# Kernel tuning notes

Measured on AMD Instinct MI355X. Metric: run time of the kernel, lower is better.

## Reference

```python
import jax, jax.numpy as jnp
import numpy as np
import math

D_MODEL = 1024
NUM_HEADS = 16
HEAD_DIM = D_MODEL // NUM_HEADS
B, T = 2, 2048


def _linear_params(key, d_in, d_out):
    kw, kb = jax.random.split(key)
    s = 1.0 / math.sqrt(d_in)
    W = jax.random.uniform(kw, (d_in, d_out), jnp.float32, -s, s)
    b = jax.random.uniform(kb, (d_out,), jnp.float32, -s, s)
    return W, b


def setup_inputs() -> dict:
    key = jax.random.key(0)
    ks = jax.random.split(key, 10)
    x_real = jax.random.normal(ks[0], (B, T, D_MODEL), jnp.float32)
    x_imag = jax.random.normal(ks[1], (B, T, D_MODEL), jnp.float32)
    Wqr, bqr = _linear_params(ks[2], D_MODEL, D_MODEL)
    Wqi, bqi = _linear_params(ks[3], D_MODEL, D_MODEL)
    Wkr, bkr = _linear_params(ks[4], D_MODEL, D_MODEL)
    Wki, bki = _linear_params(ks[5], D_MODEL, D_MODEL)
    Wvr, bvr = _linear_params(ks[6], D_MODEL, D_MODEL)
    Wvi, bvi = _linear_params(ks[7], D_MODEL, D_MODEL)
    Wor, bor = _linear_params(ks[8], D_MODEL, D_MODEL)
    Woi, boi = _linear_params(ks[9], D_MODEL, D_MODEL)
    return dict(x_real=x_real, x_imag=x_imag,
                Wqr=Wqr, bqr=bqr, Wqi=Wqi, bqi=bqi,
                Wkr=Wkr, bkr=bkr, Wki=Wki, bki=bki,
                Wvr=Wvr, bvr=bvr, Wvi=Wvi, bvi=bvi,
                Wor=Wor, bor=bor, Woi=Woi, boi=boi)


def _heads(x):
    # (B,T,C) -> (B,H,T,Dh)
    b, t, _ = x.shape
    return x.reshape(b, t, NUM_HEADS, HEAD_DIM).transpose(0, 2, 1, 3)


def reference(x_real, x_imag,
              Wqr, bqr, Wqi, bqi, Wkr, bkr, Wki, bki,
              Wvr, bvr, Wvi, bvi, Wor, bor, Woi, boi):
    b, t, c = x_real.shape
    # NOTE: first two qr/qi assignments in the torch forward are dead code;
    # effective math is below.
    qr = _heads(x_real @ Wqr + bqr)
    qi = _heads(x_imag @ Wqi + bqi)
    kr = _heads(x_real @ Wkr + bkr)
    ki = _heads(x_imag @ Wki + bki)
    vr = _heads(x_real @ Wvr + bvr)
    vi = _heads(x_imag @ Wvi + bvi)
    # Re(Q K^H) score: Qr*Kr + Qi*Ki, scaled
    score = (jnp.einsum('bhtd,bhsd->bhts', qr, kr)
             + jnp.einsum('bhtd,bhsd->bhts', qi, ki)) / math.sqrt(HEAD_DIM)
    causal = jnp.triu(jnp.ones((t, t), dtype=bool), k=1)  # True above diagonal
    score = jnp.where(causal[None, None], -jnp.inf, score)
    attn = jax.nn.softmax(score, axis=-1)
    out_r = jnp.einsum('bhts,bhsd->bhtd', attn, vr).transpose(0, 2, 1, 3).reshape(b, t, c)
    out_i = jnp.einsum('bhts,bhsd->bhtd', attn, vi).transpose(0, 2, 1, 3).reshape(b, t, c)
    final_r = out_r @ Wor + bor
    final_i = out_i @ Woi + boi
    return (final_r, final_i)
```

## Files before the change

kernel.cpp:

```cpp
#include <hip/hip_runtime.h>
#include <hip/hip_bf16.h>


typedef __attribute__((ext_vector_type(8))) __bf16 bf16x8;
typedef __attribute__((ext_vector_type(4))) float f32x4;
typedef unsigned short u16;

#define L2E 1.44269504088896340736f

__device__ __forceinline__ void gl2lds16(const void* g, void* l) {
  __builtin_amdgcn_global_load_lds(
      (const __attribute__((address_space(1))) unsigned int*)g,
      (__attribute__((address_space(3))) unsigned int*)l, 16, 0, 0);
}

__device__ __forceinline__ u16 f2bf(float f) {
  union { float f; unsigned u; } v;
  v.f = f;
  unsigned r = v.u + 0x7FFFu + ((v.u >> 16) & 1u);
  return (u16)(r >> 16);
}

__global__ void cvt_bf16_2(const float* __restrict__ a, const float* __restrict__ bsrc,
                           u16* __restrict__ oa, u16* __restrict__ ob, int n) {
  const float* in = blockIdx.y ? bsrc : a;
  u16* out = blockIdx.y ? ob : oa;
  int stride = gridDim.x * blockDim.x * 4;
  for (int i = (blockIdx.x * blockDim.x + threadIdx.x) * 4; i < n; i += stride) {
    float4 v = *(const float4*)(in + i);
    ushort4 o;
    o.x = f2bf(v.x); o.y = f2bf(v.y); o.z = f2bf(v.z); o.w = f2bf(v.w);
    *(ushort4*)(out + i) = o;
  }
}

struct WPtrs { const float* w[8]; };

__global__ void cvt_w_t(WPtrs ptrs, u16* __restrict__ out) {
  __shared__ float tile[32][33];
  const float* W = ptrs.w[blockIdx.z];
  u16* o = out + ((size_t)blockIdx.z << 20);
  int tx = threadIdx.x & 31, ty = threadIdx.x >> 5;
  int bx = blockIdx.x * 32, by = blockIdx.y * 32;
#pragma unroll
  for (int k = 0; k < 4; k++) {
    int r = by + ty + k * 8;
    tile[ty + k * 8][tx] = W[(size_t)r * 1024 + bx + tx];
  }
  __syncthreads();
#pragma unroll
  for (int k = 0; k < 4; k++) {
    int n = bx + ty + k * 8;
    o[(size_t)n * 1024 + by + tx] = f2bf(tile[tx][ty + k * 8]);
  }
}

struct GemmArgs {
  const u16* A[6];
  const u16* Wt[6];
  const float* bias[6];
  void* dst[6];
  int off[6];
  int vt[6];
  float scale[6];
};

template <int MODE>
__global__ __launch_bounds__(256, 2) void gemm_bf16(GemmArgs args) {
  extern __shared__ u16 dynpad[];
  const int z = blockIdx.z;
  const u16* __restrict__ A = args.A[z];
  const u16* __restrict__ Bt = args.Wt[z];
  const float* __restrict__ bias = args.bias[z];
  const int brow = blockIdx.x * 128;
  const int bcol = blockIdx.y * 128;

  __shared__ u16 smem[2][2][128 * 32];

  const int tid = threadIdx.x;
  const int w = tid >> 6, lane = tid & 63;
  const int ql = lane & 15, hi = lane >> 4;
  const int wrow = (w >> 1) * 64, wcol = (w & 1) * 64;

  if (args.off[z] == -12345) ((volatile u16*)dynpad)[0] = 0;

  f32x4 acc[4][4] = {};

  auto stage = [&](int buf, int t) {
    int k0 = t * 32;
#pragma unroll
    for (int s = 0; s < 2; s++) {
      int q = w * 2 + s;
      int lr = q * 16 + (lane >> 2);
      int csrc = (lane & 3) ^ ((lr >> 1) & 3);
      gl2lds16(A + (size_t)(brow + lr) * 1024 + k0 + csrc * 8, &smem[0][buf][q * 512]);
    }
#pragma unroll
    for (int s = 0; s < 2; s++) {
      int q = w * 2 + s;
      int lr = q * 16 + (lane >> 2);
      int csrc = (lane & 3) ^ ((lr >> 1) & 3);
      gl2lds16(Bt + (size_t)(bcol + lr) * 1024 + k0 + csrc * 8, &smem[1][buf][q * 512]);
    }
  };

  stage(0, 0);
  __syncthreads();

  int buf = 0;
  for (int t = 0; t < 32; t++) {
    if (t + 1 < 32) stage(buf ^ 1, t + 1);
    bf16x8 a[4], b[4];
#pragma unroll
    for (int i = 0; i < 4; i++) {
      int row = wrow + i * 16 + ql;
      int cs = hi ^ ((row >> 1) & 3);
      a[i] = *(const bf16x8*)&smem[0][buf][row * 32 + cs * 8];
      int col = wcol + i * 16 + ql;
      int cs2 = hi ^ ((col >> 1) & 3);
      b[i] = *(const bf16x8*)&smem[1][buf][col * 32 + cs2 * 8];
    }
#pragma unroll
    for (int i = 0; i < 4; i++)
#pragma unroll
      for (int j = 0; j < 4; j++)
        acc[i][j] = __builtin_amdgcn_mfma_f32_16x16x32_bf16(a[i], b[j], acc[i][j], 0, 0, 0);
    __syncthreads();
    buf ^= 1;
  }

  const int off = args.off[z];
  const float scl = args.scale[z];

  if (MODE == 1 && args.vt[z]) {
    u16* sm = &smem[0][0][0];
    const int bb = brow >> 11, t0 = brow & 2047;
    const int h0 = bcol >> 6;
    u16* dstV = (u16*)args.dst[z];
#pragma unroll
    for (int p = 0; p < 2; p++) {
      if ((w & 1) == p) {
#pragma unroll
        for (int i = 0; i < 4; i++)
#pragma unroll
          for (int j = 0; j < 4; j++) {
            int col_local = j * 16 + ql;
            int row_base = wrow + i * 16 + hi * 4;
            float bv = bias[bcol + p * 64 + col_local];
            union { __bf16 hh[4]; uint2 u; } cv;
#pragma unroll
            for (int r = 0; r < 4; r++) cv.hh[r] = (__bf16)((acc[i][j][r] + bv) * scl);
            *(uint2*)&sm[col_local * 136 + row_base] = cv.u;
          }
      }
      __syncthreads();
      {
        int dh = tid >> 2, tq = tid & 3;
        const u16* src = &sm[dh * 136 + tq * 32];
        u16* dp = dstV + ((size_t)((bb * 16 + h0 + p) * 128) + off + dh) * 2048 + t0 + tq * 32;
#pragma unroll
        for (int k = 0; k < 4; k++)
          *(uint4*)(dp + k * 8) = *(const uint4*)(src + k * 8);
      }
      __syncthreads();
    }
    return;
  }

#pragma unroll
  for (int i = 0; i < 4; i++)
#pragma unroll
    for (int j = 0; j < 4; j++)
#pragma unroll
      for (int r = 0; r < 4; r++) {
        int grow = brow + wrow + i * 16 + hi * 4 + r;
        int gcol = bcol + wcol + j * 16 + ql;
        float v = (acc[i][j][r] + bias[gcol]) * scl;
        if (MODE == 0) {
          ((float*)args.dst[z])[(size_t)grow * 1024 + gcol] = v;
        } else {
          int bb = grow >> 11, tt = grow & 2047;
          int h = gcol >> 6, dh = gcol & 63;
          ((u16*)args.dst[z])[(((size_t)(bb * 16 + h) * 2048 + tt) << 7) + off + dh] = f2bf(v);
        }
      }
}

__global__ __launch_bounds__(256, 2) void attn_kernel(
    const u16* __restrict__ Q, const u16* __restrict__ K, const u16* __restrict__ Vt,
    u16* __restrict__ Or, u16* __restrict__ Oi) {
  const int bh = blockIdx.x;
  const int ii = (int)gridDim.y - 1 - (int)blockIdx.y;
  const int tid = threadIdx.x, w = tid >> 6, lane = tid & 63;
  const int ql = lane & 15, hi = lane >> 4;
  const int b = bh >> 4, h = bh & 15;

  __shared__ u16 lK[2][64 * 128];
  __shared__ u16 lV[2][128 * 64];
  __shared__ u16 lP[4][16 * 64];

  const int qrow0 = ii * 64 + w * 16;
  const int q = qrow0 + ql;

  bf16x8 qf[4];
#pragma unroll
  for (int kk = 0; kk < 4; kk++)
    qf[kk] = *(const bf16x8*)(Q + ((size_t)bh * 2048 + q) * 128 + kk * 32 + hi * 8);

  f32x4 o[8] = {};
  float l = 0.f;

  const int ntiles = ii + 1;

  auto stageKV = [&](int buf, int jt) {
#pragma unroll
    for (int s = 0; s < 4; s++) {
      int seg = w * 4 + s;
      int srow = seg * 4 + (lane >> 4);
      int csrc = (lane & 15) ^ (srow & 15);
      gl2lds16(K + ((size_t)bh * 2048 + jt * 64 + srow) * 128 + csrc * 8, &lK[buf][seg * 512]);
    }
#pragma unroll
    for (int s = 0; s < 4; s++) {
      int seg = w * 4 + s;
      int dv = seg * 8 + (lane >> 3);
      int csrc = (lane & 7) ^ (dv & 7);
      gl2lds16(Vt + ((size_t)bh * 128 + dv) * 2048 + jt * 64 + csrc * 8, &lV[buf][seg * 512]);
    }
  };

  stageKV(0, 0);
  __syncthreads();

  int buf = 0;
  for (int jt = 0; jt < ntiles; jt++) {
    if (jt + 1 < ntiles) stageKV(buf ^ 1, jt + 1);

    f32x4 s[4] = {};
    __builtin_amdgcn_s_setprio(1);
#pragma unroll
    for (int kk = 0; kk < 4; kk++) {
#pragma unroll
      for (int j = 0; j < 4; j++) {
        int sl = j * 16 + ql;
        int cs = (kk * 4 + hi) ^ (sl & 15);
        bf16x8 kf = *(const bf16x8*)&lK[buf][sl * 128 + cs * 8];
        s[j] = __builtin_amdgcn_mfma_f32_16x16x32_bf16(kf, qf[kk], s[j], 0, 0, 0);
      }
    }
    __builtin_amdgcn_s_setprio(0);

    if (jt == ii) {
#pragma unroll
      for (int j = 0; j < 4; j++)
#pragma unroll
        for (int r = 0; r < 4; r++) {
          int kg = jt * 64 + j * 16 + hi * 4 + r;
          if (kg > q) s[j][r] = -__builtin_inff();
        }
    }

    uint2 pk[4];
#pragma unroll
    for (int j = 0; j < 4; j++) {
      float p0 = exp2f(__builtin_fmaf(s[j][0], L2E, -16.f * L2E));
      float p1 = exp2f(__builtin_fmaf(s[j][1], L2E, -16.f * L2E));
      float p2 = exp2f(__builtin_fmaf(s[j][2], L2E, -16.f * L2E));
      float p3 = exp2f(__builtin_fmaf(s[j][3], L2E, -16.f * L2E));
      l += (p0 + p1) + (p2 + p3);
      union { __bf16 hh[4]; uint2 u; } cv;
      cv.hh[0] = (__bf16)p0; cv.hh[1] = (__bf16)p1;
      cv.hh[2] = (__bf16)p2; cv.hh[3] = (__bf16)p3;
      pk[j] = cv.u;
    }

#pragma unroll
    for (int j = 0; j < 4; j++) {
      int byte_off = ql * 128 + ((j * 32 + hi * 8) ^ ((ql & 7) << 4));
      *(uint2*)((char*)&lP[w][0] + byte_off) = pk[j];
    }
    asm volatile("s_waitcnt lgkmcnt(0)" ::: "memory");
    __builtin_amdgcn_sched_barrier(0);

    __builtin_amdgcn_s_setprio(1);
#pragma unroll
    for (int kks = 0; kks < 2; kks++) {
      int pb = ql * 128 + ((kks * 64 + hi * 16) ^ ((ql & 7) << 4));
      bf16x8 pf = *(const bf16x8*)((char*)&lP[w][0] + pb);
#pragma unroll
      for (int jv = 0; jv < 8; jv++) {
        int dv = jv * 16 + ql;
        int cs = (kks * 4 + hi) ^ (dv & 7);
        bf16x8 vf = *(const bf16x8*)&lV[buf][dv * 64 + cs * 8];
        o[jv] = __builtin_amdgcn_mfma_f32_16x16x32_bf16(vf, pf, o[jv], 0, 0, 0);
      }
    }
    __builtin_amdgcn_s_setprio(0);

    __syncthreads();
    buf ^= 1;
  }

  l += __shfl_xor(l, 16);
  l += __shfl_xor(l, 32);
  float linv = 1.f / l;
  const size_t obase = ((size_t)b * 2048 + q) * 1024 + h * 64;
#pragma unroll
  for (int jv = 0; jv < 8; jv++) {
    ushort4 st;
    union { __bf16 hh[4]; ushort4 u; } cv;
    cv.hh[0] = (__bf16)(o[jv][0] * linv);
    cv.hh[1] = (__bf16)(o[jv][1] * linv);
    cv.hh[2] = (__bf16)(o[jv][2] * linv);
    cv.hh[3] = (__bf16)(o[jv][3] * linv);
    st = cv.u;
    u16* dst = (jv < 4) ? Or : Oi;
    *(ushort4*)(dst + obase + (jv & 3) * 16 + hi * 4) = st;
  }
}

extern "C" void kernel_launch(void* const* d_in, const int* in_sizes, int n_in,
                              void* d_out, int out_size, void* d_ws, size_t ws_size,
                              hipStream_t stream) {
  (void)in_sizes; (void)n_in; (void)out_size; (void)ws_size;

  const float* x_real = (const float*)d_in[0];
  const float* x_imag = (const float*)d_in[1];

  char* ws = (char*)d_ws;
  size_t off = 0;
  auto alloc = [&](size_t bytes) {
    void* p = ws + off;
    off += (bytes + 255) & ~(size_t)255;
    return p;
  };
  const size_t MK = 4096ull * 1024;
  u16* xr16 = (u16*)alloc(MK * 2);
  u16* xi16 = (u16*)alloc(MK * 2);
  u16* Wt   = (u16*)alloc(8ull * 1024 * 1024 * 2);
  u16* Qc   = (u16*)alloc(32ull * 2048 * 128 * 2);
  u16* Kc   = (u16*)alloc(32ull * 2048 * 128 * 2);
  u16* Vt   = (u16*)alloc(32ull * 2048 * 128 * 2);
  u16* Or   = (u16*)alloc(MK * 2);
  u16* Oi   = (u16*)alloc(MK * 2);

  cvt_bf16_2<<<dim3(1024, 2), 256, 0, stream>>>(x_real, x_imag, xr16, xi16, (int)MK);

  WPtrs wp;
  wp.w[0] = (const float*)d_in[2];
  wp.w[1] = (const float*)d_in[4];
  wp.w[2] = (const float*)d_in[6];
  wp.w[3] = (const float*)d_in[8];
  wp.w[4] = (const float*)d_in[10];
  wp.w[5] = (const float*)d_in[12];
  wp.w[6] = (const float*)d_in[14];
  wp.w[7] = (const float*)d_in[16];
  cvt_w_t<<<dim3(32, 32, 8), 256, 0, stream>>>(wp, Wt);

  GemmArgs pa{};
  const u16* xs[2] = {xr16, xi16};
  for (int z = 0; z < 6; z++) {
    pa.A[z] = xs[z & 1];
    pa.Wt[z] = Wt + (size_t)z * 1048576;
    pa.off[z] = (z & 1) * 64;
    pa.vt[z] = (z >= 4) ? 1 : 0;
    pa.scale[z] = (z < 2) ? 0.125f : 1.0f;
  }
  pa.bias[0] = (const float*)d_in[3];
  pa.bias[1] = (const float*)d_in[5];
  pa.bias[2] = (const float*)d_in[7];
  pa.bias[3] = (const float*)d_in[9];
  pa.bias[4] = (const float*)d_in[11];
  pa.bias[5] = (const float*)d_in[13];
  pa.dst[0] = Qc; pa.dst[1] = Qc;
  pa.dst[2] = Kc; pa.dst[3] = Kc;
  pa.dst[4] = Vt; pa.dst[5] = Vt;
  gemm_bf16<1><<<dim3(32, 8, 6), 256, 16384, stream>>>(pa);

  attn_kernel<<<dim3(32, 32), 256, 0, stream>>>(Qc, Kc, Vt, Or, Oi);

  GemmArgs fa{};
  fa.A[0] = Or; fa.A[1] = Oi;
  fa.Wt[0] = Wt + 6ull * 1048576;
  fa.Wt[1] = Wt + 7ull * 1048576;
  fa.bias[0] = (const float*)d_in[15];
  fa.bias[1] = (const float*)d_in[17];
  fa.dst[0] = (float*)d_out;
  fa.dst[1] = (float*)d_out + MK;
  fa.off[0] = 0; fa.off[1] = 0;
  fa.vt[0] = 0; fa.vt[1] = 0;
  fa.scale[0] = 1.0f; fa.scale[1] = 1.0f;
  gemm_bf16<0><<<dim3(32, 8, 2), 256, 16384, stream>>>(fa);
}
```

Before: 175.6 us.

## Pair causal query tiles per block to balance work and share K/V loads

```diff
diff --git a/kernel.cpp b/kernel.cpp
--- a/kernel.cpp
+++ b/kernel.cpp
@@ -190,27 +190,30 @@
     const u16* __restrict__ Q, const u16* __restrict__ K, const u16* __restrict__ Vt,
     u16* __restrict__ Or, u16* __restrict__ Oi) {
   const int bh = blockIdx.x;
-  const int ii = (int)gridDim.y - 1 - (int)blockIdx.y;
+  const int p = blockIdx.y;
+  const int iiA = p, iiB = 31 - p;
   const int tid = threadIdx.x, w = tid >> 6, lane = tid & 63;
   const int ql = lane & 15, hi = lane >> 4;
   const int b = bh >> 4, h = bh & 15;
 
   __shared__ u16 lK[2][64 * 128];
   __shared__ u16 lV[2][128 * 64];
-  __shared__ u16 lP[4][16 * 64];
-
-  const int qrow0 = ii * 64 + w * 16;
-  const int q = qrow0 + ql;
-
-  bf16x8 qf[4];
-#pragma unroll
-  for (int kk = 0; kk < 4; kk++)
-    qf[kk] = *(const bf16x8*)(Q + ((size_t)bh * 2048 + q) * 128 + kk * 32 + hi * 8);
-
-  f32x4 o[8] = {};
-  float l = 0.f;
-
-  const int ntiles = ii + 1;
+  __shared__ u16 lP[8][16 * 64];
+
+  const int qA = iiA * 64 + w * 16 + ql;
+  const int qB = iiB * 64 + w * 16 + ql;
+
+  bf16x8 qfA[4], qfB[4];
+#pragma unroll
+  for (int kk = 0; kk < 4; kk++) {
+    qfA[kk] = *(const bf16x8*)(Q + ((size_t)bh * 2048 + qA) * 128 + kk * 32 + hi * 8);
+    qfB[kk] = *(const bf16x8*)(Q + ((size_t)bh * 2048 + qB) * 128 + kk * 32 + hi * 8);
+  }
+
+  f32x4 oA[8] = {}, oB[8] = {};
+  float lsA = 0.f, lsB = 0.f;
+
+  const int ntiles = iiB + 1;
 
   auto stageKV = [&](int buf, int jt) {
 #pragma unroll
@@ -235,64 +238,112 @@
   int buf = 0;
   for (int jt = 0; jt < ntiles; jt++) {
     if (jt + 1 < ntiles) stageKV(buf ^ 1, jt + 1);
-
-    f32x4 s[4] = {};
+    const bool doA = (jt <= iiA);
+
+    f32x4 sA[4] = {}, sB[4] = {};
     __builtin_amdgcn_s_setprio(1);
-#pragma unroll
-    for (int kk = 0; kk < 4; kk++) {
-#pragma unroll
-      for (int j = 0; j < 4; j++) {
-        int sl = j * 16 + ql;
-        int cs = (kk * 4 + hi) ^ (sl & 15);
-        bf16x8 kf = *(const bf16x8*)&lK[buf][sl * 128 + cs * 8];
-        s[j] = __builtin_amdgcn_mfma_f32_16x16x32_bf16(kf, qf[kk], s[j], 0, 0, 0);
-      }
+    if (doA) {
+#pragma unroll
+      for (int kk = 0; kk < 4; kk++)
+#pragma unroll
+        for (int j = 0; j < 4; j++) {
+          int sl = j * 16 + ql;
+          int cs = (kk * 4 + hi) ^ (sl & 15);
+          bf16x8 kf = *(const bf16x8*)&lK[buf][sl * 128 + cs * 8];
+          sB[j] = __builtin_amdgcn_mfma_f32_16x16x32_bf16(kf, qfB[kk], sB[j], 0, 0, 0);
+          sA[j] = __builtin_amdgcn_mfma_f32_16x16x32_bf16(kf, qfA[kk], sA[j], 0, 0, 0);
+        }
+    } else {
+#pragma unroll
+      for (int kk = 0; kk < 4; kk++)
+#pragma unroll
+        for (int j = 0; j < 4; j++) {
+          int sl = j * 16 + ql;
+          int cs = (kk * 4 + hi) ^ (sl & 15);
+          bf16x8 kf = *(const bf16x8*)&lK[buf][sl * 128 + cs * 8];
+          sB[j] = __builtin_amdgcn_mfma_f32_16x16x32_bf16(kf, qfB[kk], sB[j], 0, 0, 0);
+        }
     }
     __builtin_amdgcn_s_setprio(0);
 
-    if (jt == ii) {
+    if (jt == iiB) {
 #pragma unroll
       for (int j = 0; j < 4; j++)
 #pragma unroll
         for (int r = 0; r < 4; r++) {
           int kg = jt * 64 + j * 16 + hi * 4 + r;
-          if (kg > q) s[j][r] = -__builtin_inff();
-        }
-    }
-
-    uint2 pk[4];
+          if (kg > qB) sB[j][r] = -__builtin_inff();
+        }
+    }
+    if (jt == iiA) {
+#pragma unroll
+      for (int j = 0; j < 4; j++)
+#pragma unroll
+        for (int r = 0; r < 4; r++) {
+          int kg = jt * 64 + j * 16 + hi * 4 + r;
+          if (kg > qA) sA[j][r] = -__builtin_inff();
+        }
+    }
+
 #pragma unroll
     for (int j = 0; j < 4; j++) {
-      float p0 = exp2f(__builtin_fmaf(s[j][0], L2E, -16.f * L2E));
-      float p1 = exp2f(__builtin_fmaf(s[j][1], L2E, -16.f * L2E));
-      float p2 = exp2f(__builtin_fmaf(s[j][2], L2E, -16.f * L2E));
-      float p3 = exp2f(__builtin_fmaf(s[j][3], L2E, -16.f * L2E));
-      l += (p0 + p1) + (p2 + p3);
+      float p0 = exp2f(__builtin_fmaf(sB[j][0], L2E, -16.f * L2E));
+      float p1 = exp2f(__builtin_fmaf(sB[j][1], L2E, -16.f * L2E));
+      float p2 = exp2f(__builtin_fmaf(sB[j][2], L2E, -16.f * L2E));
+      float p3 = exp2f(__builtin_fmaf(sB[j][3], L2E, -16.f * L2E));
+      lsB += (p0 + p1) + (p2 + p3);
       union { __bf16 hh[4]; uint2 u; } cv;
       cv.hh[0] = (__bf16)p0; cv.hh[1] = (__bf16)p1;
       cv.hh[2] = (__bf16)p2; cv.hh[3] = (__bf16)p3;
-      pk[j] = cv.u;
-    }
-
-#pragma unroll
-    for (int j = 0; j < 4; j++) {
       int byte_off = ql * 128 + ((j * 32 + hi * 8) ^ ((ql & 7) << 4));
-      *(uint2*)((char*)&lP[w][0] + byte_off) = pk[j];
+      *(uint2*)((char*)&lP[w * 2][0] + byte_off) = cv.u;
+    }
+    if (doA) {
+#pragma unroll
+      for (int j = 0; j < 4; j++) {
+        float p0 = exp2f(__builtin_fmaf(sA[j][0], L2E, -16.f * L2E));
+        float p1 = exp2f(__builtin_fmaf(sA[j][1], L2E, -16.f * L2E));
+        float p2 = exp2f(__builtin_fmaf(sA[j][2], L2E, -16.f * L2E));
+        float p3 = exp2f(__builtin_fmaf(sA[j][3], L2E, -16.f * L2E));
+        lsA += (p0 + p1) + (p2 + p3);
+        union { __bf16 hh[4]; uint2 u; } cv;
+        cv.hh[0] = (__bf16)p0; cv.hh[1] = (__bf16)p1;
+        cv.hh[2] = (__bf16)p2; cv.hh[3] = (__bf16)p3;
+        int byte_off = ql * 128 + ((j * 32 + hi * 8) ^ ((ql & 7) << 4));
+        *(uint2*)((char*)&lP[w * 2 + 1][0] + byte_off) = cv.u;
+      }
     }
     asm volatile("s_waitcnt lgkmcnt(0)" ::: "memory");
     __builtin_amdgcn_sched_barrier(0);
 
     __builtin_amdgcn_s_setprio(1);
-#pragma unroll
-    for (int kks = 0; kks < 2; kks++) {
-      int pb = ql * 128 + ((kks * 64 + hi * 16) ^ ((ql & 7) << 4));
-      bf16x8 pf = *(const bf16x8*)((char*)&lP[w][0] + pb);
-#pragma unroll
-      for (int jv = 0; jv < 8; jv++) {
-        int dv = jv * 16 + ql;
-        int cs = (kks * 4 + hi) ^ (dv & 7);
-        bf16x8 vf = *(const bf16x8*)&lV[buf][dv * 64 + cs * 8];
-        o[jv] = __builtin_amdgcn_mfma_f32_16x16x32_bf16(vf, pf, o[jv], 0, 0, 0);
+    if (doA) {
+#pragma unroll
+      for (int kks = 0; kks < 2; kks++) {
+        int pb = ql * 128 + ((kks * 64 + hi * 16) ^ ((ql & 7) << 4));
+        bf16x8 pfB = *(const bf16x8*)((char*)&lP[w * 2][0] + pb);
+        bf16x8 pfA = *(const bf16x8*)((char*)&lP[w * 2 + 1][0] + pb);
+#pragma unroll
+        for (int jv = 0; jv < 8; jv++) {
+          int dv = jv * 16 + ql;
+          int cs = (kks * 4 + hi) ^ (dv & 7);
+          bf16x8 vf = *(const bf16x8*)&lV[buf][dv * 64 + cs * 8];
+          oB[jv] = __builtin_amdgcn_mfma_f32_16x16x32_bf16(vf, pfB, oB[jv], 0, 0, 0);
+          oA[jv] = __builtin_amdgcn_mfma_f32_16x16x32_bf16(vf, pfA, oA[jv], 0, 0, 0);
+        }
+      }
+    } else {
+#pragma unroll
+      for (int kks = 0; kks < 2; kks++) {
+        int pb = ql * 128 + ((kks * 64 + hi * 16) ^ ((ql & 7) << 4));
+        bf16x8 pfB = *(const bf16x8*)((char*)&lP[w * 2][0] + pb);
+#pragma unroll
+        for (int jv = 0; jv < 8; jv++) {
+          int dv = jv * 16 + ql;
+          int cs = (kks * 4 + hi) ^ (dv & 7);
+          bf16x8 vf = *(const bf16x8*)&lV[buf][dv * 64 + cs * 8];
+          oB[jv] = __builtin_amdgcn_mfma_f32_16x16x32_bf16(vf, pfB, oB[jv], 0, 0, 0);
+        }
       }
     }
     __builtin_amdgcn_s_setprio(0);
@@ -301,21 +352,24 @@
     buf ^= 1;
   }
 
-  l += __shfl_xor(l, 16);
-  l += __shfl_xor(l, 32);
-  float linv = 1.f / l;
-  const size_t obase = ((size_t)b * 2048 + q) * 1024 + h * 64;
+  lsB += __shfl_xor(lsB, 16);
+  lsB += __shfl_xor(lsB, 32);
+  lsA += __shfl_xor(lsA, 16);
+  lsA += __shfl_xor(lsA, 32);
+  float invB = 1.f / lsB, invA = 1.f / lsA;
+  const size_t obaseB = ((size_t)b * 2048 + qB) * 1024 + h * 64;
+  const size_t obaseA = ((size_t)b * 2048 + qA) * 1024 + h * 64;
 #pragma unroll
   for (int jv = 0; jv < 8; jv++) {
-    ushort4 st;
-    union { __bf16 hh[4]; ushort4 u; } cv;
-    cv.hh[0] = (__bf16)(o[jv][0] * linv);
-    cv.hh[1] = (__bf16)(o[jv][1] * linv);
-    cv.hh[2] = (__bf16)(o[jv][2] * linv);
-    cv.hh[3] = (__bf16)(o[jv][3] * linv);
-    st = cv.u;
+    union { __bf16 hh[4]; ushort4 u; } cvB, cvA;
+#pragma unroll
+    for (int r = 0; r < 4; r++) {
+      cvB.hh[r] = (__bf16)(oB[jv][r] * invB);
+      cvA.hh[r] = (__bf16)(oA[jv][r] * invA);
+    }
     u16* dst = (jv < 4) ? Or : Oi;
-    *(ushort4*)(dst + obase + (jv & 3) * 16 + hi * 4) = st;
+    *(ushort4*)(dst + obaseB + (jv & 3) * 16 + hi * 4) = cvB.u;
+    *(ushort4*)(dst + obaseA + (jv & 3) * 16 + hi * 4) = cvA.u;
   }
 }
 
@@ -377,7 +431,7 @@
   pa.dst[4] = Vt; pa.dst[5] = Vt;
   gemm_bf16<1><<<dim3(32, 8, 6), 256, 16384, stream>>>(pa);
 
-  attn_kernel<<<dim3(32, 32), 256, 0, stream>>>(Qc, Kc, Vt, Or, Oi);
+  attn_kernel<<<dim3(32, 16), 256, 0, stream>>>(Qc, Kc, Vt, Or, Oi);
 
   GemmArgs fa{};
   fa.A[0] = Or; fa.A[1] = Oi;
```

New measurement: 193.0 us. 9.9% more time.

## Restructure attention kernel to 32x32 MFMA with split-KV waves and LDS reduction

Applied to the files above, without the earlier changes.

```diff
diff --git a/kernel.cpp b/kernel.cpp
--- a/kernel.cpp
+++ b/kernel.cpp
@@ -4,9 +4,12 @@
 
 typedef __attribute__((ext_vector_type(8))) __bf16 bf16x8;
 typedef __attribute__((ext_vector_type(4))) float f32x4;
+typedef __attribute__((ext_vector_type(16))) float f32x16;
 typedef unsigned short u16;
+typedef unsigned int u32;
 
 #define L2E 1.44269504088896340736f
+#define NEG16L2E (-23.0831207542234f)
 
 __device__ __forceinline__ void gl2lds16(const void* g, void* l) {
   __builtin_amdgcn_global_load_lds(
@@ -19,6 +22,12 @@
   v.f = f;
   unsigned r = v.u + 0x7FFFu + ((v.u >> 16) & 1u);
   return (u16)(r >> 16);
+}
+
+__device__ __forceinline__ u32 cvtpk(float lo, float hi) {
+  u32 d;
+  asm("v_cvt_pk_bf16_f32 %0, %1, %2" : "=v"(d) : "v"(lo), "v"(hi));
+  return d;
 }
 
 __global__ void cvt_bf16_2(const float* __restrict__ a, const float* __restrict__ bsrc,
@@ -192,130 +201,154 @@
   const int bh = blockIdx.x;
   const int ii = (int)gridDim.y - 1 - (int)blockIdx.y;
   const int tid = threadIdx.x, w = tid >> 6, lane = tid & 63;
-  const int ql = lane & 15, hi = lane >> 4;
-  const int b = bh >> 4, h = bh & 15;
-
-  __shared__ u16 lK[2][64 * 128];
-  __shared__ u16 lV[2][128 * 64];
-  __shared__ u16 lP[4][16 * 64];
-
-  const int qrow0 = ii * 64 + w * 16;
-  const int q = qrow0 + ql;
-
-  bf16x8 qf[4];
-#pragma unroll
-  for (int kk = 0; kk < 4; kk++)
-    qf[kk] = *(const bf16x8*)(Q + ((size_t)bh * 2048 + q) * 128 + kk * 32 + hi * 8);
-
-  f32x4 o[8] = {};
+  const int q32 = lane & 31;
+  const int hb = lane >> 5;
+  const int wq = w & 1, wk = w >> 1;
+  const int b = bh >> 4, hh = bh & 15;
+
+  __shared__ u16 lK[128 * 128];
+  __shared__ u16 lV[128 * 128];
+  __shared__ u16 lP[4][32 * 64];
+
+  const int q = ii * 64 + wq * 32 + q32;
+
+  bf16x8 qf[8];
+#pragma unroll
+  for (int kk = 0; kk < 8; kk++)
+    qf[kk] = *(const bf16x8*)(Q + ((size_t)bh * 2048 + q) * 128 + kk * 16 + hb * 8);
+
+  f32x16 o[4] = {};
   float l = 0.f;
 
-  const int ntiles = ii + 1;
-
-  auto stageKV = [&](int buf, int jt) {
-#pragma unroll
-    for (int s = 0; s < 4; s++) {
-      int seg = w * 4 + s;
-      int srow = seg * 4 + (lane >> 4);
+  const int nIter = (ii + 2) >> 1;
+
+  for (int jt = 0; jt < nIter; jt++) {
+#pragma unroll
+    for (int s8 = 0; s8 < 8; s8++) {
+      int op = w * 8 + s8;
+      int srow = op * 4 + (lane >> 4);
       int csrc = (lane & 15) ^ (srow & 15);
-      gl2lds16(K + ((size_t)bh * 2048 + jt * 64 + srow) * 128 + csrc * 8, &lK[buf][seg * 512]);
-    }
-#pragma unroll
-    for (int s = 0; s < 4; s++) {
-      int seg = w * 4 + s;
-      int dv = seg * 8 + (lane >> 3);
-      int csrc = (lane & 7) ^ (dv & 7);
-      gl2lds16(Vt + ((size_t)bh * 128 + dv) * 2048 + jt * 64 + csrc * 8, &lV[buf][seg * 512]);
-    }
-  };
-
-  stageKV(0, 0);
+      gl2lds16(K + ((size_t)bh * 2048 + jt * 128 + srow) * 128 + csrc * 8, &lK[op * 512]);
+    }
+#pragma unroll
+    for (int s8 = 0; s8 < 8; s8++) {
+      int op = w * 8 + s8;
+      int dv = op * 4 + (lane >> 4);
+      int csrc = (lane & 15) ^ (dv & 15);
+      gl2lds16(Vt + ((size_t)bh * 128 + dv) * 2048 + jt * 128 + csrc * 8, &lV[op * 512]);
+    }
+    asm volatile("s_waitcnt vmcnt(0)" ::: "memory");
+    __syncthreads();
+
+    if (jt * 128 + wk * 64 <= ii * 64 + wq * 32 + 31) {
+      f32x16 s0 = {}, s1 = {};
+      __builtin_amdgcn_s_setprio(1);
+#pragma unroll
+      for (int kk = 0; kk < 8; kk++) {
+        int ch = kk * 2 + hb;
+        int r0 = wk * 64 + q32;
+        int r1 = r0 + 32;
+        bf16x8 kf0 = *(const bf16x8*)&lK[r0 * 128 + (ch ^ (r0 & 15)) * 8];
+        bf16x8 kf1 = *(const bf16x8*)&lK[r1 * 128 + (ch ^ (r1 & 15)) * 8];
+        s0 = __builtin_amdgcn_mfma_f32_32x32x16_bf16(kf0, qf[kk], s0, 0, 0, 0);
+        s1 = __builtin_amdgcn_mfma_f32_32x32x16_bf16(kf1, qf[kk], s1, 0, 0, 0);
+      }
+      __builtin_amdgcn_s_setprio(0);
+
+      if (jt * 128 + wk * 64 + 63 > ii * 64 + wq * 32) {
+#pragma unroll
+        for (int reg = 0; reg < 16; reg++) {
+          int krow = (reg & 3) + 8 * (reg >> 2) + 4 * hb;
+          int k0g = jt * 128 + wk * 64 + krow;
+          if (k0g > q) s0[reg] = -1e30f;
+          if (k0g + 32 > q) s1[reg] = -1e30f;
+        }
+      }
+
+#pragma unroll
+      for (int j2 = 0; j2 < 2; j2++)
+#pragma unroll
+        for (int rq = 0; rq < 4; rq++) {
+          float p0, p1, p2, p3;
+          if (j2 == 0) {
+            p0 = exp2f(__builtin_fmaf(s0[rq * 4 + 0], L2E, NEG16L2E));
+            p1 = exp2f(__builtin_fmaf(s0[rq * 4 + 1], L2E, NEG16L2E));
+            p2 = exp2f(__builtin_fmaf(s0[rq * 4 + 2], L2E, NEG16L2E));
+            p3 = exp2f(__builtin_fmaf(s0[rq * 4 + 3], L2E, NEG16L2E));
+          } else {
+            p0 = exp2f(__builtin_fmaf(s1[rq * 4 + 0], L2E, NEG16L2E));
+            p1 = exp2f(__builtin_fmaf(s1[rq * 4 + 1], L2E, NEG16L2E));
+            p2 = exp2f(__builtin_fmaf(s1[rq * 4 + 2], L2E, NEG16L2E));
+            p3 = exp2f(__builtin_fmaf(s1[rq * 4 + 3], L2E, NEG16L2E));
+          }
+          l += (p0 + p1) + (p2 + p3);
+          int g = j2 * 4 + rq;
+          int byte_off = q32 * 128 + ((g ^ (q32 & 7)) * 16) + hb * 8;
+          uint2 pk2;
+          pk2.x = cvtpk(p0, p1);
+          pk2.y = cvtpk(p2, p3);
+          *(uint2*)((char*)&lP[w][0] + byte_off) = pk2;
+        }
+      asm volatile("s_waitcnt lgkmcnt(0)" ::: "memory");
+      __builtin_amdgcn_sched_barrier(0);
+
+      __builtin_amdgcn_s_setprio(1);
+#pragma unroll
+      for (int kk2 = 0; kk2 < 4; kk2++) {
+        int G = kk2 * 2 + hb;
+        bf16x8 pf = *(const bf16x8*)((char*)&lP[w][0] + q32 * 128 + ((G ^ (q32 & 7)) * 16));
+#pragma unroll
+        for (int jv2 = 0; jv2 < 4; jv2++) {
+          int dv = jv2 * 32 + q32;
+          int ch = wk * 8 + kk2 * 2 + hb;
+          bf16x8 vf = *(const bf16x8*)&lV[dv * 128 + (ch ^ (dv & 15)) * 8];
+          o[jv2] = __builtin_amdgcn_mfma_f32_32x32x16_bf16(vf, pf, o[jv2], 0, 0, 0);
+        }
+      }
+      __builtin_amdgcn_s_setprio(0);
+    }
+
+    __syncthreads();
+  }
+
+  l += __shfl_xor(l, 32);
+  float* mO = (float*)&lK[0];
+  float* mL = (float*)&lV[0];
+
+  if (w >= 2) {
+#pragma unroll
+    for (int jv2 = 0; jv2 < 4; jv2++)
+#pragma unroll
+      for (int rq = 0; rq < 4; rq++) {
+        int dvb = jv2 * 32 + rq * 8 + 4 * hb;
+        int dvs = (dvb + 4 * q32) & 127;
+        f32x4 t;
+        t[0] = o[jv2][rq * 4 + 0]; t[1] = o[jv2][rq * 4 + 1];
+        t[2] = o[jv2][rq * 4 + 2]; t[3] = o[jv2][rq * 4 + 3];
+        *(f32x4*)&mO[(w - 2) * 4096 + q32 * 128 + dvs] = t;
+      }
+    if (lane < 32) mL[(w - 2) * 32 + q32] = l;
+  }
   __syncthreads();
 
-  int buf = 0;
-  for (int jt = 0; jt < ntiles; jt++) {
-    if (jt + 1 < ntiles) stageKV(buf ^ 1, jt + 1);
-
-    f32x4 s[4] = {};
-    __builtin_amdgcn_s_setprio(1);
-#pragma unroll
-    for (int kk = 0; kk < 4; kk++) {
-#pragma unroll
-      for (int j = 0; j < 4; j++) {
-        int sl = j * 16 + ql;
-        int cs = (kk * 4 + hi) ^ (sl & 15);
-        bf16x8 kf = *(const bf16x8*)&lK[buf][sl * 128 + cs * 8];
-        s[j] = __builtin_amdgcn_mfma_f32_16x16x32_bf16(kf, qf[kk], s[j], 0, 0, 0);
-      }
-    }
-    __builtin_amdgcn_s_setprio(0);
-
-    if (jt == ii) {
-#pragma unroll
-      for (int j = 0; j < 4; j++)
-#pragma unroll
-        for (int r = 0; r < 4; r++) {
-          int kg = jt * 64 + j * 16 + hi * 4 + r;
-          if (kg > q) s[j][r] = -__builtin_inff();
-        }
-    }
-
-    uint2 pk[4];
-#pragma unroll
-    for (int j = 0; j < 4; j++) {
-      float p0 = exp2f(__builtin_fmaf(s[j][0], L2E, -16.f * L2E));
-      float p1 = exp2f(__builtin_fmaf(s[j][1], L2E, -16.f * L2E));
-      float p2 = exp2f(__builtin_fmaf(s[j][2], L2E, -16.f * L2E));
-      float p3 = exp2f(__builtin_fmaf(s[j][3], L2E, -16.f * L2E));
-      l += (p0 + p1) + (p2 + p3);
-      union { __bf16 hh[4]; uint2 u; } cv;
-      cv.hh[0] = (__bf16)p0; cv.hh[1] = (__bf16)p1;
-      cv.hh[2] = (__bf16)p2; cv.hh[3] = (__bf16)p3;
-      pk[j] = cv.u;
-    }
-
-#pragma unroll
-    for (int j = 0; j < 4; j++) {
-      int byte_off = ql * 128 + ((j * 32 + hi * 8) ^ ((ql & 7) << 4));
-      *(uint2*)((char*)&lP[w][0] + byte_off) = pk[j];
-    }
-    asm volatile("s_waitcnt lgkmcnt(0)" ::: "memory");
-    __builtin_amdgcn_sched_barrier(0);
-
-    __builtin_amdgcn_s_setprio(1);
-#pragma unroll
-    for (int kks = 0; kks < 2; kks++) {
-      int pb = ql * 128 + ((kks * 64 + hi * 16) ^ ((ql & 7) << 4));
-      bf16x8 pf = *(const bf16x8*)((char*)&lP[w][0] + pb);
-#pragma unroll
-      for (int jv = 0; jv < 8; jv++) {
-        int dv = jv * 16 + ql;
-        int cs = (kks * 4 + hi) ^ (dv & 7);
-        bf16x8 vf = *(const bf16x8*)&lV[buf][dv * 64 + cs * 8];
-        o[jv] = __builtin_amdgcn_mfma_f32_16x16x32_bf16(vf, pf, o[jv], 0, 0, 0);
-      }
-    }
-    __builtin_amdgcn_s_setprio(0);
-
-    __syncthreads();
-    buf ^= 1;
-  }
-
-  l += __shfl_xor(l, 16);
-  l += __shfl_xor(l, 32);
-  float linv = 1.f / l;
-  const size_t obase = ((size_t)b * 2048 + q) * 1024 + h * 64;
-#pragma unroll
-  for (int jv = 0; jv < 8; jv++) {
-    ushort4 st;
-    union { __bf16 hh[4]; ushort4 u; } cv;
-    cv.hh[0] = (__bf16)(o[jv][0] * linv);
-    cv.hh[1] = (__bf16)(o[jv][1] * linv);
-    cv.hh[2] = (__bf16)(o[jv][2] * linv);
-    cv.hh[3] = (__bf16)(o[jv][3] * linv);
-    st = cv.u;
-    u16* dst = (jv < 4) ? Or : Oi;
-    *(ushort4*)(dst + obase + (jv & 3) * 16 + hi * 4) = st;
+  if (w < 2) {
+    float lt = l + mL[w * 32 + q32];
+    float linv = 1.f / lt;
+    const size_t obase = ((size_t)b * 2048 + q) * 1024 + hh * 64;
+#pragma unroll
+    for (int jv2 = 0; jv2 < 4; jv2++)
+#pragma unroll
+      for (int rq = 0; rq < 4; rq++) {
+        int dvb = jv2 * 32 + rq * 8 + 4 * hb;
+        int dvs = (dvb + 4 * q32) & 127;
+        f32x4 part = *(const f32x4*)&mO[w * 4096 + q32 * 128 + dvs];
+        union { __bf16 hh4[4]; ushort4 u; } cv;
+#pragma unroll
+        for (int r = 0; r < 4; r++)
+          cv.hh4[r] = (__bf16)((o[jv2][rq * 4 + r] + part[r]) * linv);
+        u16* dst = (jv2 < 2) ? Or : Oi;
+        *(ushort4*)(dst + obase + (jv2 & 1) * 32 + rq * 8 + 4 * hb) = cv.u;
+      }
   }
 }
 
```

Result: no change. 175.1 us, median of 2 (-0.3%).
